# Optimization experiments

Measured on AMD Instinct MI355X. Metric: run time of the kernel, lower is better.

The kernel has to match this reference:

```python
import jax, jax.numpy as jnp
import numpy as np

# Config mirrors Voxelization(__init__) with training=True -> max_voxels[0]
VOXEL_SIZE = (0.05, 0.05, 0.1)
PC_LO = (0.0, -40.0, -3.0)
PC_HI = (70.4, 40.0, 1.0)
MAX_POINTS = 64
MAX_VOXELS = 60000
GX = int(round((PC_HI[0] - PC_LO[0]) / VOXEL_SIZE[0]))  # 1408
GY = int(round((PC_HI[1] - PC_LO[1]) / VOXEL_SIZE[1]))  # 1600
GZ = int(round((PC_HI[2] - PC_LO[2]) / VOXEL_SIZE[2]))  # 40
SENT = GX * GY * GZ  # sentinel linear id for out-of-range points


def setup_inputs() -> dict:
    key = jax.random.key(0)
    u = jax.random.uniform(key, (2_000_000, 4), dtype=jnp.float32)
    lo = jnp.array([PC_LO[0], PC_LO[1], PC_LO[2], 0.0], jnp.float32)
    span = jnp.array([PC_HI[0] - PC_LO[0], PC_HI[1] - PC_LO[1], PC_HI[2] - PC_LO[2], 1.0], jnp.float32)
    points = lo + u * span  # xyz inside range, intensity in [0,1)
    return {"points": points}


def _voxelize(points):
    N, C = points.shape
    vs = jnp.array(VOXEL_SIZE, jnp.float32)
    lo = jnp.array(PC_LO, jnp.float32)
    grid = jnp.array([GX, GY, GZ], jnp.int32)

    g = jnp.floor((points[:, :3] - lo) / vs).astype(jnp.int32)  # [N,3] grid coords (x,y,z)
    valid = jnp.all((g >= 0) & (g < grid), axis=1)
    lin = (g[:, 0] * GY + g[:, 1]) * GZ + g[:, 2]
    lin = jnp.where(valid, lin, SENT).astype(jnp.int32)

    # Stable sort by voxel id; ties keep original point order (deterministic mode)
    order = jnp.argsort(lin)  # jnp.argsort is stable
    sl = lin[order]
    idx = jnp.arange(N, dtype=jnp.int32)
    is_start = jnp.concatenate([jnp.ones((1,), bool), sl[1:] != sl[:-1]])
    gid_sorted = (jnp.cumsum(is_start) - 1).astype(jnp.int32)  # sorted-group id per sorted point

    # First original point index per group -> first-occurrence voxel ordering
    group_first = jnp.full((N,), N, jnp.int32).at[gid_sorted].min(
        jnp.where(is_start, order.astype(jnp.int32), N))
    group_lin = jnp.full((N,), SENT, jnp.int32).at[gid_sorted].min(sl)
    group_first = jnp.where(group_lin == SENT, N, group_first)  # sentinel group ranks last
    perm = jnp.argsort(group_first)  # rank -> group
    inv_rank = jnp.zeros((N,), jnp.int32).at[perm].set(idx)  # group -> rank

    num_valid = jnp.sum(is_start & (sl != SENT)).astype(jnp.int32)
    voxel_num = jnp.minimum(num_valid, MAX_VOXELS)

    # Position within voxel (point order within group)
    start_idx = jax.lax.cummax(jnp.where(is_start, idx, -1))
    pos_sorted = idx - start_idx

    gid = jnp.zeros((N,), jnp.int32).at[order].set(gid_sorted)
    pos = jnp.zeros((N,), jnp.int32).at[order].set(pos_sorted)
    rank = inv_rank[gid]
    keep = valid & (rank < MAX_VOXELS) & (pos < MAX_POINTS)
    rk = jnp.where(keep, rank, MAX_VOXELS)  # OOB -> dropped
    pk = jnp.where(keep, pos, MAX_POINTS)

    voxels = jnp.zeros((MAX_VOXELS, MAX_POINTS, C), points.dtype).at[rk, pk].set(points, mode='drop')
    coors = jnp.zeros((MAX_VOXELS, 3), jnp.int32).at[rk].set(g[:, ::-1], mode='drop')  # flip -> (z,y,x)
    group_count = jnp.zeros((N,), jnp.int32).at[gid_sorted].add((sl != SENT).astype(jnp.int32))
    npv = jnp.minimum(group_count[perm], MAX_POINTS)[:MAX_VOXELS].astype(jnp.int32)
    return voxels, coors, npv, voxel_num


def reference(points):
    # Padded equivalent of torch output (voxels[:n], coors[:n].flip(-1), npv[:n]):
    # rows >= voxel_num are zero; voxel_num gives the true count.
    return _voxelize(points)
```

## Files before the change

### kernel.cpp

```cpp
#include <hip/hip_runtime.h>


#define MAXV 60000
#define MAXP 64
#define FCUT 131072
#define NBUCK 512
#define BSHIFT 13
#define BSLOTS 8192
#define TMASK (NBUCK * BSLOTS - 1)
#define BCAP 5120
#define ECAP 512
#define BIN_CHUNK 4096
#define BIN_T 512
#define CHUNK 2048
#define NCHUNK (FCUT / CHUNK)

typedef unsigned long long u64;

__device__ __forceinline__ int compute_lin(float x, float y, float z) {
  float fx = floorf((x - 0.0f) / 0.05f);
  float fy = floorf((y - (-40.0f)) / 0.05f);
  float fz = floorf((z - (-3.0f)) / 0.1f);
  if (!(fx >= 0.0f && fx < 1408.0f &&
        fy >= 0.0f && fy < 1600.0f &&
        fz >= 0.0f && fz < 40.0f))
    return -1;
  return (((int)fx) * 1600 + (int)fy) * 40 + (int)fz;
}

__device__ __forceinline__ unsigned hash_s(int lin) {
  unsigned h = (unsigned)lin * 2654435761u;
  return (h ^ (h >> 15)) & TMASK;
}

__global__ __launch_bounds__(BIN_T) void k_binA(const float4* __restrict__ pts,
                                                int N, u64* __restrict__ binned,
                                                int* __restrict__ bucketCnt) {
  __shared__ int hist[NBUCK];
  __shared__ int lbase[NBUCK];
  __shared__ int cursor[NBUCK];
  __shared__ int gbase[NBUCK];
  __shared__ int totSh;
  __shared__ u64 stage[BIN_CHUNK];

  int tid = threadIdx.x;
  int blockStart = blockIdx.x * BIN_CHUNK;
  hist[tid] = 0;
  __syncthreads();

  unsigned sArr[8];
  int linArr[8];
#pragma unroll
  for (int j = 0; j < 8; j++) {
    int i = blockStart + j * BIN_T + tid;
    unsigned sv = 0xFFFFFFFFu; int lv = 0;
    if (i < N) {
      float4 p = pts[i];
      int lin = compute_lin(p.x, p.y, p.z);
      if (lin >= 0) {
        sv = hash_s(lin);
        lv = lin;
        atomicAdd(&hist[sv >> BSHIFT], 1);
      }
    }
    sArr[j] = sv; linArr[j] = lv;
  }
  __syncthreads();

  int v = hist[tid];
  lbase[tid] = v;
  __syncthreads();
  for (int off = 1; off < NBUCK; off <<= 1) {
    int t = (tid >= off) ? lbase[tid - off] : 0;
    __syncthreads();
    lbase[tid] += t;
    __syncthreads();
  }
  int excl = lbase[tid] - v;
  __syncthreads();
  lbase[tid] = excl;
  cursor[tid] = excl;
  __syncthreads();

#pragma unroll
  for (int j = 0; j < 8; j++) {
    if (sArr[j] != 0xFFFFFFFFu) {
      int b = (int)(sArr[j] >> BSHIFT);
      int k = atomicAdd(&cursor[b], 1);
      int i = blockStart + j * BIN_T + tid;
      stage[k] = ((u64)(unsigned)linArr[j] << 32) | (unsigned)i;
    }
  }
  __syncthreads();

  int cntB = cursor[tid] - lbase[tid];
  if (cntB > 0) gbase[tid] = atomicAdd(&bucketCnt[tid], cntB);
  if (tid == BIN_T - 1) totSh = cursor[NBUCK - 1];
  __syncthreads();

  int tot = totSh;
  for (int k = tid; k < tot; k += BIN_T) {
    u64 e = stage[k];
    int b = (int)(hash_s((int)(e >> 32)) >> BSHIFT);
    int off = gbase[b] + (k - lbase[b]);
    if (off < BCAP) binned[(size_t)b * BCAP + off] = e;
  }
}

__global__ __launch_bounds__(1024) void k_binB(
    const u64* __restrict__ binned, const int* __restrict__ bucketCnt,
    u64* __restrict__ fs, u64* __restrict__ gEbuf, int* __restrict__ bcnt,
    int* __restrict__ occPartials) {
  __shared__ u64 tab[BSLOTS];
  __shared__ u64 ev[ECAP];
  __shared__ int evCnt;
  __shared__ int occTot;

  int tid = threadIdx.x;
  int b = blockIdx.x;
  for (int k = tid; k < BSLOTS / 2; k += 1024)
    ((ulonglong2*)tab)[k] = make_ulonglong2(~0ull, ~0ull);
  if (tid == 0) { evCnt = 0; occTot = 0; }
  __syncthreads();

  int n = bucketCnt[b]; if (n > BCAP) n = BCAP;
  for (int k = tid; k < n; k += 1024) {
    u64 e = binned[(size_t)b * BCAP + k];
    int i = (int)(unsigned)e;
    int lin = (int)(e >> 32);
    int ls = (int)(hash_s(lin) & (BSLOTS - 1));
    u64 mine = ((u64)(unsigned)i << 40) | ((u64)(unsigned)lin << 12);
    for (;;) {
      u64 cur = atomicCAS(&tab[ls], ~0ull, mine);
      if (cur == ~0ull) break;
      if (((cur >> 12) & 0xFFFFFFFull) == (u64)(unsigned)lin) {
        for (;;) {
          unsigned f = (unsigned)(cur >> 40);
          unsigned c = (unsigned)(cur & 0xFFFu);
          unsigned nf = ((unsigned)i < f) ? (unsigned)i : f;
          unsigned rec = ((unsigned)i < f) ? f : (unsigned)i;
          unsigned nc = (c < 0xFFFu) ? c + 1 : 0xFFFu;
          u64 nv = ((u64)nf << 40) | ((u64)(unsigned)lin << 12) | nc;
          u64 prev = atomicCAS(&tab[ls], cur, nv);
          if (prev == cur) {
            unsigned pos = c + 1;
            if (pos < MAXP) {
              int eidx = atomicAdd(&evCnt, 1);
              if (eidx < ECAP)
                ev[eidx] = ((u64)ls << 40) | ((u64)pos << 24) | rec;
            }
            break;
          }
          cur = prev;
        }
        break;
      }
      ls = (ls + 1) & (BSLOTS - 1);
    }
  }
  __syncthreads();

  int ec = evCnt; if (ec > ECAP) ec = ECAP;
  for (int k = tid; k < ec; k += 1024) {
    u64 e = ev[k];
    int ls = (int)(e >> 40);
    u64 pm = (e >> 24) & 0xFFFFull;
    unsigned rec = (unsigned)(e & 0xFFFFFFu);
    unsigned f = (unsigned)(tab[ls] >> 40);
    gEbuf[(size_t)b * ECAP + k] =
        (f < FCUT) ? (((u64)f << 40) | (pm << 24) | rec) : ~0ull;
  }
  if (tid == 0) bcnt[b] = ec;

  int occ = 0;
  for (int k = tid; k < BSLOTS / 2; k += 1024) {
    ulonglong2 w2 = ((const ulonglong2*)tab)[k];
#pragma unroll
    for (int h = 0; h < 2; h++) {
      u64 w = h ? w2.y : w2.x;
      if (w != ~0ull) {
        occ++;
        unsigned f = (unsigned)(w >> 40);
        if (f < FCUT) {
          unsigned lin = (unsigned)((w >> 12) & 0xFFFFFFFull);
          unsigned c = (unsigned)(w & 0xFFFu) + 1;
          if (c > MAXP) c = MAXP;
          fs[f] = ((u64)lin << 8) | c;
        }
      }
    }
  }
  for (int off = 32; off > 0; off >>= 1) occ += __shfl_down(occ, off);
  if ((tid & 63) == 0) atomicAdd(&occTot, occ);
  __syncthreads();
  if (tid == 0) occPartials[b] = occTot;
}

__global__ __launch_bounds__(256) void k_rankLB(
    const u64* __restrict__ fs, const float4* __restrict__ pts,
    const int* __restrict__ occPartials, int* __restrict__ status,
    int* __restrict__ rankOf,
    float* __restrict__ outCoors, float* __restrict__ outNpv,
    float4* __restrict__ outVox, float* __restrict__ outNum,
    int* __restrict__ Dws) {
  int b = blockIdx.x;
  int tid = threadIdx.x;
  int base = b * CHUNK + tid * 8;
  __shared__ int sd[256];
  __shared__ int exclSh;

  u64 v[8];
  int sum = 0;
#pragma unroll
  for (int j = 0; j < 8; j++) {
    v[j] = fs[base + j];
    sum += (v[j] != 0) ? 1 : 0;
  }
  sd[tid] = sum;
  __syncthreads();
  for (int off = 1; off < 256; off <<= 1) {
    int t = (tid >= off) ? sd[tid - off] : 0;
    __syncthreads();
    sd[tid] += t;
    __syncthreads();
  }
  int inclThread = sd[tid];

  if (tid == 255)
    __hip_atomic_store(&status[b], 0x40000000 | inclThread,
                       __ATOMIC_RELEASE, __HIP_MEMORY_SCOPE_AGENT);

  int myAgg = 0;
  if (tid < b) {
    int sv;
    do {
      sv = __hip_atomic_load(&status[tid], __ATOMIC_ACQUIRE,
                             __HIP_MEMORY_SCOPE_AGENT);
    } while (!(sv & 0x40000000));
    myAgg = sv & 0x3FFFFFFF;
  }
  for (int off = 32; off > 0; off >>= 1) myAgg += __shfl_down(myAgg, off);
  if (tid == 0) exclSh = myAgg;
  __syncthreads();

  int run = exclSh + inclThread - sum;
#pragma unroll
  for (int j = 0; j < 8; j++) {
    if (v[j] != 0) {
      int f = base + j;
      int r = run++;
      rankOf[f] = r;
      if (r < MAXV) {
        int lin = (int)(v[j] >> 8);
        int gz = lin % 40;
        int t = lin / 40;
        int gy = t % 1600;
        int gx = t / 1600;
        outCoors[r * 3 + 0] = (float)gz;
        outCoors[r * 3 + 1] = (float)gy;
        outCoors[r * 3 + 2] = (float)gx;
        outNpv[r] = (float)(int)(v[j] & 0xFF);
        outVox[(size_t)r * MAXP] = pts[f];
      }
    }
  }

  if (b == 0) {
    int acc = 0;
    for (int i = tid; i < NBUCK; i += 256) acc += occPartials[i];
    __syncthreads();
    sd[tid] = acc;
    __syncthreads();
    for (int off = 128; off > 0; off >>= 1) {
      if (tid < off) sd[tid] += sd[tid + off];
      __syncthreads();
    }
    if (tid == 0) {
      int D = sd[0];
      int vn = D < MAXV ? D : MAXV;
      outNum[0] = (float)vn;
      Dws[0] = vn;
    }
  }
}

__global__ void k_events(const float4* __restrict__ pts,
                         const int* __restrict__ bcnt,
                         const u64* __restrict__ gEbuf,
                         const int* __restrict__ rankOf,
                         const int* __restrict__ Dws,
                         float* __restrict__ outCoors,
                         float* __restrict__ outNpv,
                         float4* __restrict__ outVox) {
  int gid = blockIdx.x * 256 + threadIdx.x;

  int D = Dws[0];
  for (int r = D + gid; r < MAXV; r += NBUCK * ECAP) {
    outCoors[r * 3 + 0] = 0.f; outCoors[r * 3 + 1] = 0.f;
    outCoors[r * 3 + 2] = 0.f; outNpv[r] = 0.f;
  }

  int b = gid >> 9;
  int t = gid & (ECAP - 1);
  if (t >= bcnt[b]) return;
  u64 e = gEbuf[(size_t)b * ECAP + t];
  if (e == ~0ull) return;
  unsigned f = (unsigned)(e >> 40);
  unsigned pos = (unsigned)((e >> 24) & 0xFFFFu);
  unsigned rec = (unsigned)(e & 0xFFFFFFu);
  int r = rankOf[f];
  if ((unsigned)r >= (unsigned)MAXV) return;
  outVox[(size_t)r * MAXP + pos] = pts[rec];
}

extern "C" void kernel_launch(void* const* d_in, const int* in_sizes, int n_in,
                              void* d_out, int out_size, void* d_ws, size_t ws_size,
                              hipStream_t stream) {
  const float4* pts = (const float4*)d_in[0];
  int N = in_sizes[0] / 4;

  float* out = (float*)d_out;
  float* outVox = out;
  float* outCoors = out + (size_t)MAXV * MAXP * 4;
  float* outNpv = outCoors + (size_t)MAXV * 3;
  float* outNum = outNpv + MAXV;

  char* w = (char*)d_ws;
  u64* binned = (u64*)w;         w += (size_t)NBUCK * BCAP * 8;
  u64* gEbuf = (u64*)w;          w += (size_t)NBUCK * ECAP * 8;
  int* rankOf = (int*)w;         w += (size_t)FCUT * 4;
  int* occPartials = (int*)w;    w += NBUCK * 4;
  int* bcnt = (int*)w;           w += NBUCK * 4;
  int* Dws = (int*)w;            w += 256;
  char* z0 = w;
  u64* fs = (u64*)w;             w += (size_t)FCUT * 8;
  int* bucketCnt = (int*)w;      w += NBUCK * 4;
  int* status = (int*)w;         w += NCHUNK * 4;
  size_t zBytes = (size_t)(w - z0);

  hipMemsetAsync(d_out, 0, (size_t)out_size * sizeof(float), stream);
  hipMemsetAsync(z0, 0, zBytes, stream);

  int nbA = (N + BIN_CHUNK - 1) / BIN_CHUNK;

  k_binA<<<nbA, BIN_T, 0, stream>>>(pts, N, binned, bucketCnt);
  k_binB<<<NBUCK, 1024, 0, stream>>>(binned, bucketCnt, fs, gEbuf, bcnt,
                                     occPartials);
  k_rankLB<<<NCHUNK, 256, 0, stream>>>(fs, pts, occPartials, status, rankOf,
                                       outCoors, outNpv, (float4*)outVox,
                                       outNum, Dws);
  k_events<<<NBUCK * ECAP / 256, 256, 0, stream>>>(pts, bcnt, gEbuf, rankOf,
                                                   Dws, outCoors, outNpv,
                                                   (float4*)outVox);
}
```

Baseline: 144.0 us.

## Fold output zeroing into binning kernel and fuse event scatter via grid barrier

The output memset and the zeroing of the fs table move into extra blocks of the binning kernel, so they can overlap with the binning work. The separate events kernel is merged into the rank kernel, joined by an atomic grid-wide spin barrier. This cuts one memset and one kernel launch. In exchange, the event gather/scatter now runs on only 64 blocks in a strided loop, and the barrier relies on all 64 blocks being co-resident.

```diff
diff --git a/kernel.cpp b/kernel.cpp
--- a/kernel.cpp
+++ b/kernel.cpp
@@ -12,6 +12,7 @@
 #define ECAP 512
 #define BIN_CHUNK 4096
 #define BIN_T 512
+#define NZ 512
 #define CHUNK 2048
 #define NCHUNK (FCUT / CHUNK)
 
@@ -33,9 +34,23 @@
   return (h ^ (h >> 15)) & TMASK;
 }
 
-__global__ __launch_bounds__(BIN_T) void k_binA(const float4* __restrict__ pts,
-                                                int N, u64* __restrict__ binned,
-                                                int* __restrict__ bucketCnt) {
+__global__ __launch_bounds__(BIN_T) void k_binA(
+    const float4* __restrict__ pts, int N, u64* __restrict__ binned,
+    int* __restrict__ bucketCnt, int nBin,
+    float4* __restrict__ zOut, int nf4, float* __restrict__ zTail, int ntail,
+    ulonglong2* __restrict__ zFs, int nfs2) {
+  int tid = threadIdx.x;
+
+  if (blockIdx.x >= nBin) {
+    int gid = (blockIdx.x - nBin) * BIN_T + tid;
+    int stride = NZ * BIN_T;
+    float4 z = make_float4(0.f, 0.f, 0.f, 0.f);
+    for (int i = gid; i < nf4; i += stride) zOut[i] = z;
+    for (int i = gid; i < nfs2; i += stride) zFs[i] = make_ulonglong2(0, 0);
+    if (gid < ntail) zTail[gid] = 0.f;
+    return;
+  }
+
   __shared__ int hist[NBUCK];
   __shared__ int lbase[NBUCK];
   __shared__ int cursor[NBUCK];
@@ -43,7 +58,6 @@
   __shared__ int totSh;
   __shared__ u64 stage[BIN_CHUNK];
 
-  int tid = threadIdx.x;
   int blockStart = blockIdx.x * BIN_CHUNK;
   hist[tid] = 0;
   __syncthreads();
@@ -199,7 +213,8 @@
 __global__ __launch_bounds__(256) void k_rankLB(
     const u64* __restrict__ fs, const float4* __restrict__ pts,
     const int* __restrict__ occPartials, int* __restrict__ status,
-    int* __restrict__ rankOf,
+    int* __restrict__ barCnt, const int* __restrict__ bcnt,
+    const u64* __restrict__ gEbuf, int* __restrict__ rankOf,
     float* __restrict__ outCoors, float* __restrict__ outNpv,
     float4* __restrict__ outVox, float* __restrict__ outNum,
     int* __restrict__ Dws) {
@@ -282,35 +297,36 @@
       Dws[0] = vn;
     }
   }
-}
-
-__global__ void k_events(const float4* __restrict__ pts,
-                         const int* __restrict__ bcnt,
-                         const u64* __restrict__ gEbuf,
-                         const int* __restrict__ rankOf,
-                         const int* __restrict__ Dws,
-                         float* __restrict__ outCoors,
-                         float* __restrict__ outNpv,
-                         float4* __restrict__ outVox) {
-  int gid = blockIdx.x * 256 + threadIdx.x;
-
-  int D = Dws[0];
-  for (int r = D + gid; r < MAXV; r += NBUCK * ECAP) {
+
+  __threadfence();
+  __syncthreads();
+  if (tid == 0) {
+    __hip_atomic_fetch_add(barCnt, 1, __ATOMIC_ACQ_REL,
+                           __HIP_MEMORY_SCOPE_AGENT);
+    while (__hip_atomic_load(barCnt, __ATOMIC_ACQUIRE,
+                             __HIP_MEMORY_SCOPE_AGENT) < NCHUNK) {}
+  }
+  __syncthreads();
+
+  int gid = b * 256 + tid;
+  int D = __hip_atomic_load(Dws, __ATOMIC_ACQUIRE, __HIP_MEMORY_SCOPE_AGENT);
+  for (int r = D + gid; r < MAXV; r += NCHUNK * 256) {
     outCoors[r * 3 + 0] = 0.f; outCoors[r * 3 + 1] = 0.f;
     outCoors[r * 3 + 2] = 0.f; outNpv[r] = 0.f;
   }
-
-  int b = gid >> 9;
-  int t = gid & (ECAP - 1);
-  if (t >= bcnt[b]) return;
-  u64 e = gEbuf[(size_t)b * ECAP + t];
-  if (e == ~0ull) return;
-  unsigned f = (unsigned)(e >> 40);
-  unsigned pos = (unsigned)((e >> 24) & 0xFFFFu);
-  unsigned rec = (unsigned)(e & 0xFFFFFFu);
-  int r = rankOf[f];
-  if ((unsigned)r >= (unsigned)MAXV) return;
-  outVox[(size_t)r * MAXP + pos] = pts[rec];
+  for (int k = gid; k < NBUCK * ECAP; k += NCHUNK * 256) {
+    int bk = k >> 9;
+    int t = k & (ECAP - 1);
+    if (t >= bcnt[bk]) continue;
+    u64 e = gEbuf[(size_t)bk * ECAP + t];
+    if (e == ~0ull) continue;
+    unsigned f = (unsigned)(e >> 40);
+    unsigned pos = (unsigned)((e >> 24) & 0xFFFFu);
+    unsigned rec = (unsigned)(e & 0xFFFFFFu);
+    int r = rankOf[f];
+    if ((unsigned)r >= (unsigned)MAXV) continue;
+    outVox[(size_t)r * MAXP + pos] = pts[rec];
+  }
 }
 
 extern "C" void kernel_launch(void* const* d_in, const int* in_sizes, int n_in,
@@ -332,24 +348,26 @@
   int* occPartials = (int*)w;    w += NBUCK * 4;
   int* bcnt = (int*)w;           w += NBUCK * 4;
   int* Dws = (int*)w;            w += 256;
+  u64* fs = (u64*)w;             w += (size_t)FCUT * 8;
   char* z0 = w;
-  u64* fs = (u64*)w;             w += (size_t)FCUT * 8;
   int* bucketCnt = (int*)w;      w += NBUCK * 4;
   int* status = (int*)w;         w += NCHUNK * 4;
+  int* barCnt = (int*)w;         w += 256;
   size_t zBytes = (size_t)(w - z0);
 
-  hipMemsetAsync(d_out, 0, (size_t)out_size * sizeof(float), stream);
   hipMemsetAsync(z0, 0, zBytes, stream);
 
   int nbA = (N + BIN_CHUNK - 1) / BIN_CHUNK;
-
-  k_binA<<<nbA, BIN_T, 0, stream>>>(pts, N, binned, bucketCnt);
+  int nf4 = out_size >> 2;
+  int ntail = out_size - (nf4 << 2);
+  float* zTail = out + ((size_t)nf4 << 2);
+
+  k_binA<<<nbA + NZ, BIN_T, 0, stream>>>(pts, N, binned, bucketCnt, nbA,
+                                         (float4*)out, nf4, zTail, ntail,
+                                         (ulonglong2*)fs, FCUT / 2);
   k_binB<<<NBUCK, 1024, 0, stream>>>(binned, bucketCnt, fs, gEbuf, bcnt,
                                      occPartials);
-  k_rankLB<<<NCHUNK, 256, 0, stream>>>(fs, pts, occPartials, status, rankOf,
-                                       outCoors, outNpv, (float4*)outVox,
-                                       outNum, Dws);
-  k_events<<<NBUCK * ECAP / 256, 256, 0, stream>>>(pts, bcnt, gEbuf, rankOf,
-                                                   Dws, outCoors, outNpv,
-                                                   (float4*)outVox);
-}
+  k_rankLB<<<NCHUNK, 256, 0, stream>>>(fs, pts, occPartials, status, barCnt,
+                                       bcnt, gEbuf, rankOf, outCoors, outNpv,
+                                       (float4*)outVox, outNum, Dws);
+}
```

Measured after the change: 165.9 us. +15.3%, slower.
